# Performance work log

Hardware: AMD Instinct MI355X
Metric: run time of the kernel (lower is better)

Reference implementation:

```python
import jax, jax.numpy as jnp
import numpy as np

N = 100_000      # atoms (nodes)
E = 1_600_000    # directed edges
F_IN = 89        # atom feature dim
H = 128          # hidden dim
P = 20_000       # polyhedra (N/P = 5 atoms each)
C = 500          # crystals (P/C = 40 polyhedra each)
OUT = 1
EPS = 1e-5


def setup_inputs() -> dict:
    key = jax.random.key(0)
    ks = jax.random.split(key, 10)
    x = jax.random.normal(ks[0], (N, F_IN), jnp.float32)
    edge_index = jax.random.randint(ks[1], (2, E), 0, N)
    # sorted segment ids guaranteeing non-empty segments (faithful to PyG Batch layout)
    batch = jnp.repeat(jnp.arange(P), N // P)          # node -> polyhedron
    crystal_ids = jnp.repeat(jnp.arange(C), P // C)    # polyhedron -> crystal
    # GCNConv weights (glorot-ish) and biases; conv0 maps 89->128, convs 1..4 map 128->128
    W0 = jax.random.normal(ks[2], (F_IN, H), jnp.float32) * (1.0 / np.sqrt(F_IN))
    Ws = jax.random.normal(ks[3], (4, H, H), jnp.float32) * (1.0 / np.sqrt(H))
    bs = jnp.zeros((5, H), jnp.float32)
    # 5 BatchNorm layers
    gammas = jnp.ones((5, H), jnp.float32)
    betas = jnp.zeros((5, H), jnp.float32)
    # predictor MLP
    Wp1 = jax.random.normal(ks[4], (H, H), jnp.float32) * (1.0 / np.sqrt(H))
    bp1 = jnp.zeros((H,), jnp.float32)
    Wp2 = jax.random.normal(ks[5], (H, OUT), jnp.float32) * (1.0 / np.sqrt(H))
    bp2 = jnp.zeros((OUT,), jnp.float32)
    return dict(x=x, edge_index=edge_index, batch=batch, crystal_ids=crystal_ids,
                W0=W0, Ws=Ws, bs=bs, gammas=gammas, betas=betas,
                Wp1=Wp1, bp1=bp1, Wp2=Wp2, bp2=bp2)


def _bn(h, g, b):
    # BatchNorm1d, training mode: biased batch statistics over nodes
    mu = jnp.mean(h, axis=0)
    var = jnp.var(h, axis=0)
    return g * (h - mu) * jax.lax.rsqrt(var + EPS) + b


def reference(x, edge_index, batch, crystal_ids, W0, Ws, bs, gammas, betas, Wp1, bp1, Wp2, bp2):
    # --- GCN normalization with self-loops (shared by all 5 convs) ---
    loops = jnp.arange(N)
    src = jnp.concatenate([edge_index[0], loops])   # [E+N]
    dst = jnp.concatenate([edge_index[1], loops])
    deg = jax.ops.segment_sum(jnp.ones_like(src, jnp.float32), dst, num_segments=N)
    dinv = jnp.where(deg > 0, jax.lax.rsqrt(deg), 0.0)
    norm = (dinv[src] * dinv[dst])[:, None]          # [E+N, 1]

    def conv(h, W, b):
        m = h @ W                                    # [N, H]
        agg = jax.ops.segment_sum(m[src] * norm, dst, num_segments=N)
        return agg + b

    h = jax.nn.relu(_bn(conv(x, W0, bs[0]), gammas[0], betas[0]))
    for i in range(4):
        h = jax.nn.relu(_bn(conv(h, Ws[i], bs[i + 1]), gammas[i + 1], betas[i + 1]))

    # global_mean_pool over polyhedra
    cnt_p = jax.ops.segment_sum(jnp.ones((N,), jnp.float32), batch, num_segments=P)
    poly = jax.ops.segment_sum(h, batch, num_segments=P) / cnt_p[:, None]

    # per-crystal mean of polyhedron reps (vectorized form of the Python loop)
    cnt_c = jax.ops.segment_sum(jnp.ones((P,), jnp.float32), crystal_ids, num_segments=C)
    crys = jax.ops.segment_sum(poly, crystal_ids, num_segments=C) / cnt_c[:, None]

    # predictor MLP (Dropout is identity at inference)
    pred = jax.nn.relu(crys @ Wp1 + bp1) @ Wp2 + bp2   # [C, 1]
    return pred
```

## Files before the change

kernel.cpp:

```cpp
#include <hip/hip_runtime.h>

#define N_ATOMS 100000
#define N_EDGES 1600000
#define F_INDIM 89
#define N_CRYS  500
#define EPSBN   1e-5f
#define DRANGE  12500
#define RBLK    250
#define NSB     400

typedef unsigned short u16;
typedef unsigned int   u32;
typedef __attribute__((ext_vector_type(8))) short short8;
typedef __attribute__((ext_vector_type(4))) float f32x4;
typedef __attribute__((ext_vector_type(4))) unsigned int u32x4;

__device__ __forceinline__ float bf2f(u16 u){ union{u32 i; float f;} v; v.i=((u32)u)<<16; return v.f; }
__device__ __forceinline__ float bflo(u32 u){ union{u32 i; float f;} v; v.i=u<<16; return v.f; }
__device__ __forceinline__ float bfhi(u32 u){ union{u32 i; float f;} v; v.i=u&0xffff0000u; return v.f; }
__device__ __forceinline__ u16 f2bf(float f){
  u32 x=__float_as_uint(f);
  return (u16)((x + 0x7fffu + ((x>>16)&1u))>>16);
}
__device__ __forceinline__ u32 pack2(float a, float b){ return (u32)f2bf(a) | ((u32)f2bf(b)<<16); }
__device__ __forceinline__ float ldf(const void* p, int i, int m){
  return m ? ((const float*)p)[i] : bf2f(((const u16*)p)[i]);
}
__device__ __forceinline__ int fpmode(const void* gammas){ return (((const u16*)gammas)[0]==0) ? 1 : 0; }

__global__ void k_count(const int* __restrict__ ei, int* __restrict__ degi){
  int r = blockIdx.x & 7;
  int e = (blockIdx.x >> 3)*256 + threadIdx.x;
  if (e >= N_EDGES) return;
  int d = __builtin_nontemporal_load(ei + N_EDGES + e);
  if ((u32)d >= N_ATOMS) d = 0;
  if (d/DRANGE != r) return;
  atomicAdd(&degi[d], 1);
}

__global__ void k_hist(const int* __restrict__ degi, int* __restrict__ hist, int* __restrict__ blockHist){
  __shared__ int lh[256];
  int t = threadIdx.x, b = blockIdx.x;
  lh[t] = 0; __syncthreads();
  if (t < RBLK){
    int dg = degi[b*RBLK + t];
    atomicAdd(&lh[dg>255?255:dg], 1);
  }
  __syncthreads();
  blockHist[b*256 + t] = lh[t];
  if (lh[t]) atomicAdd(&hist[(b/50)*256 + t], lh[t]);
}

__global__ void k_hist_scan(int* __restrict__ hist){
  __shared__ int s[256];
  int R = blockIdx.x, t = threadIdx.x;
  int own = hist[R*256+t]; s[t] = own; __syncthreads();
  for (int k=1;k<256;k<<=1){ int a=(t>=k)?s[t-k]:0; __syncthreads(); s[t]+=a; __syncthreads(); }
  hist[R*256+t] = s[t] - own;
}

__global__ __launch_bounds__(64) void k_blockoff(const int* __restrict__ blockHist, const int* __restrict__ binBase,
                                                 int* __restrict__ blockOff){
  int bid = blockIdx.x;
  int c = bid & 255, R = bid >> 8;
  int t = threadIdx.x;
  int own = (t<50) ? blockHist[(R*50+t)*256 + c] : 0;
  int v = own;
  #pragma unroll
  for (int k=1;k<64;k<<=1){ int u = __shfl_up(v, k, 64); if (t>=k) v += u; }
  if (t<50) blockOff[(R*50+t)*256 + c] = R*DRANGE + binBase[R*256 + c] + (v - own);
}

__global__ void k_rank(const int* __restrict__ degi, const int* __restrict__ blockOff,
                       int* __restrict__ nodeAt, int* __restrict__ rankOf,
                       float* __restrict__ dinv, float* __restrict__ dinvR){
  __shared__ int boff[256];
  __shared__ int cnt[256];
  int b = blockIdx.x, t = threadIdx.x;
  boff[t] = blockOff[b*256 + t];
  cnt[t] = 0;
  __syncthreads();
  if (t >= RBLK) return;
  int n = b*RBLK + t;
  int dg = degi[n];
  int cd = dg>255?255:dg;
  int li = atomicAdd(&cnt[cd], 1);
  int r = boff[cd] + li;
  nodeAt[r] = n; rankOf[n] = r;
  float di = rsqrtf((float)(dg + 1));
  dinv[n] = di; dinvR[r] = di;
}

__global__ __launch_bounds__(256) void k_scan_partial(const int* __restrict__ degi, const int* __restrict__ nodeAt,
                                                      int* __restrict__ bsum){
  int b=blockIdx.x, t=threadIdx.x;
  int s=0;
  #pragma unroll
  for (int j=0;j<4;j++){
    int i=b*1024 + j*256 + t;
    if(i<N_ATOMS){
      int dg = degi[nodeAt[i]];
      s += (dg+3)&~3;
    }
  }
  __shared__ int red[256];
  red[t]=s; __syncthreads();
  for (int k=128;k>0;k>>=1){ if(t<k) red[t]+=red[t+k]; __syncthreads(); }
  if (t==0) bsum[b]=red[0];
}

__global__ void k_scan_bsum(int* __restrict__ bsum, int nb){
  __shared__ int s[128];
  int t=threadIdx.x;
  int own = (t<nb)? bsum[t]:0;
  s[t]=own; __syncthreads();
  for (int k=1;k<128;k<<=1){ int a=(t>=k)?s[t-k]:0; __syncthreads(); s[t]+=a; __syncthreads(); }
  if (t<nb) bsum[t]=s[t]-own;
}

__global__ __launch_bounds__(256) void k_scan_write(const int* __restrict__ degi, const int* __restrict__ nodeAt,
                                                    const int* __restrict__ bsum,
                                                    int* __restrict__ off, u32* __restrict__ csrS){
  int b=blockIdx.x, t=threadIdx.x;
  int base=b*1024+t*4;
  int v[4], s=0;
  #pragma unroll
  for (int j=0;j<4;j++){ int i=base+j; v[j]=(i<N_ATOMS)?((degi[nodeAt[i]]+3)&~3):0; s+=v[j]; }
  __shared__ int ts[256];
  ts[t]=s; __syncthreads();
  for (int k=1;k<256;k<<=1){ int a=(t>=k)?ts[t-k]:0; __syncthreads(); ts[t]+=a; __syncthreads(); }
  int run = ts[t]-s + bsum[b];
  #pragma unroll
  for (int j=0;j<4;j++){
    int i=base+j;
    if (i<=N_ATOMS) off[i]=run;
    if (i<N_ATOMS){
      int dg = degi[nodeAt[i]];
      for (int q=dg; q<v[j]; q++) csrS[run+q] = (u32)N_ATOMS;
    }
    run+=v[j];
  }
}

__global__ void k_fill(const int* __restrict__ ei, const int* __restrict__ off,
                       const int* __restrict__ rankOf,
                       int* __restrict__ cursor, u32* __restrict__ csrS){
  int rr = blockIdx.x & 7;
  int e = (blockIdx.x >> 3)*256 + threadIdx.x;
  if (e >= N_EDGES) return;
  int d = __builtin_nontemporal_load(ei + N_EDGES + e);
  if ((u32)d >= N_ATOMS) d = 0;
  if (d/DRANGE != rr) return;
  int s = __builtin_nontemporal_load(ei + e);
  if ((u32)s >= N_ATOMS) s = 0;
  int rk = rankOf[d];
  int p = off[rk] + atomicAdd(&cursor[rk], 1);
  csrS[p] = (u32)s;
}

__global__ void k_packW(const void* __restrict__ W0, const void* __restrict__ Ws,
                        const void* __restrict__ gammas, u16* __restrict__ dst){
  int L    = blockIdx.x >> 3;
  int tid  = (blockIdx.x & 7)*256 + threadIdx.x;
  int K    = (L==0) ? F_INDIM : 128;
  int Kpad = (L==0) ? 96 : 128;
  if (tid >= (Kpad/32)*8*64) return;
  const void* W = (L==0) ? W0 : Ws;
  int woff = (L==0) ? 0 : (L-1)*128*128;
  int fp32m = fpmode(gammas);
  int lane = tid & 63, sc = tid >> 6;
  int c = sc & 7, s = sc >> 3;
  u16 vals[8];
  #pragma unroll
  for (int j=0;j<8;j++){
    int k  = s*32 + (lane>>4)*8 + j;
    int ch = c*16 + (lane&15);
    float v = (k<K) ? ldf(W, woff + k*128 + ch, fp32m) : 0.f;
    vals[j] = f2bf(v);
  }
  u16* out = dst + (size_t)L*16384;
  *(ushort4*)&out[tid*8]   = *(const ushort4*)&vals[0];
  *(ushort4*)&out[tid*8+4] = *(const ushort4*)&vals[4];
}

#define AROW 136
__global__ __launch_bounds__(256) void k_gemm_mfma(const u16* __restrict__ inA, const void* __restrict__ inX,
                                                   int K, int Kpad, const u16* __restrict__ Wpk,
                                                   const float* __restrict__ statsPrev, int useAct,
                                                   const float* __restrict__ dinv,
                                                   u16* __restrict__ mout,
                                                   const void* __restrict__ gammas,
                                                   const void* __restrict__ betas, int goff){
  __shared__ __align__(16) u16 Al[128*AROW];
  __shared__ float cl[256];
  const int t = threadIdx.x, lane = t & 63, w = t >> 6;
  const int tile = blockIdx.x * 128;

  if (useAct){
    if (t < 128){
      int fp32m = fpmode(gammas);
      float mu  = statsPrev[t] * (1.f/N_ATOMS);
      float var = statsPrev[128+t] * (1.f/N_ATOMS) - mu*mu;
      if (var < 0.f) var = 0.f;
      float sc = ldf(gammas, goff+t, fp32m) / sqrtf(var + EPSBN);
      cl[t]     = sc;
      cl[128+t] = ldf(betas, goff+t, fp32m) - sc*mu;
    }
    __syncthreads();
    const uint4* HA4 = (const uint4*)inA;
    for (int idx=t; idx<128*16; idx+=256){
      int node = idx>>4, q = idx&15;
      int gn = tile+node;
      uint4 v = (gn<N_ATOMS) ? HA4[((size_t)(q>>2)*(N_ATOMS+1) + gn)*4 + (q&3)] : make_uint4(0,0,0,0);
      int kk = q*8;
      u16 r[8];
      r[0]=f2bf(fmaxf(fmaf(cl[kk+0], bflo(v.x), cl[128+kk+0]),0.f));
      r[1]=f2bf(fmaxf(fmaf(cl[kk+1], bfhi(v.x), cl[128+kk+1]),0.f));
      r[2]=f2bf(fmaxf(fmaf(cl[kk+2], bflo(v.y), cl[128+kk+2]),0.f));
      r[3]=f2bf(fmaxf(fmaf(cl[kk+3], bfhi(v.y), cl[128+kk+3]),0.f));
      r[4]=f2bf(fmaxf(fmaf(cl[kk+4], bflo(v.z), cl[128+kk+4]),0.f));
      r[5]=f2bf(fmaxf(fmaf(cl[kk+5], bfhi(v.z), cl[128+kk+5]),0.f));
      r[6]=f2bf(fmaxf(fmaf(cl[kk+6], bflo(v.w), cl[128+kk+6]),0.f));
      r[7]=f2bf(fmaxf(fmaf(cl[kk+7], bfhi(v.w), cl[128+kk+7]),0.f));
      *(uint4*)&Al[node*AROW + kk] = *(const uint4*)&r[0];
    }
  } else {
    int fp32m = fpmode(gammas);
    for (int idx=t; idx<128*96; idx+=256){
      int node = idx/96, kk = idx - node*96;
      int gn = tile+node;
      float v = (kk<K && gn<N_ATOMS) ? ldf(inX, gn*K+kk, fp32m) : 0.f;
      Al[node*AROW + kk] = f2bf(v);
    }
  }
  __syncthreads();

  f32x4 acc[2][8];
  #pragma unroll
  for (int rr=0;rr<2;rr++)
    #pragma unroll
    for (int c=0;c<8;c++) acc[rr][c] = (f32x4){0.f,0.f,0.f,0.f};
  const int row = lane & 15, quad = lane >> 4;

  const int nstep = Kpad >> 5;
  for (int s=0; s<nstep; ++s){
    short8 a0 = *(const short8*)&Al[(w*32+row)*AROW    + s*32 + quad*8];
    short8 a1 = *(const short8*)&Al[(w*32+16+row)*AROW + s*32 + quad*8];
    #pragma unroll
    for (int c=0;c<8;c++){
      short8 b = *(const short8*)&Wpk[(size_t)((s*8+c)*64 + lane)*8];
      acc[0][c] = __builtin_amdgcn_mfma_f32_16x16x32_bf16(a0, b, acc[0][c], 0, 0, 0);
      acc[1][c] = __builtin_amdgcn_mfma_f32_16x16x32_bf16(a1, b, acc[1][c], 0, 0, 0);
    }
  }
  __syncthreads();
  float di[2][4];
  #pragma unroll
  for (int rr=0;rr<2;rr++)
    #pragma unroll
    for (int r=0;r<4;r++){
      int gn = tile + w*32 + rr*16 + quad*4 + r;
      di[rr][r] = (gn<N_ATOMS) ? dinv[gn] : 0.f;
    }
  #pragma unroll
  for (int rr=0;rr<2;rr++)
    #pragma unroll
    for (int c=0;c<8;c++)
      #pragma unroll
      for (int r=0;r<4;r++){
        int node = w*32 + rr*16 + quad*4 + r, ch = c*16 + row;
        Al[node*AROW + ch] = f2bf(di[rr][r]*acc[rr][c][r]);
      }
  __syncthreads();
  for (int idx=t; idx<2048; idx+=256){
    int blk = idx>>9, rem = idx&511, node = rem>>2, part = rem&3;
    int gn = tile+node;
    if (gn < N_ATOMS){
      uint4 v = *(const uint4*)&Al[node*AROW + blk*32 + part*8];
      *(uint4*)&mout[((size_t)blk*(N_ATOMS+1) + gn)*32 + part*8] = v;
    }
  }
  if (blockIdx.x == gridDim.x-1 && t < 16){
    int blk = t>>2, part = t&3;
    *(uint4*)&mout[((size_t)blk*(N_ATOMS+1) + N_ATOMS)*32 + part*8] = make_uint4(0,0,0,0);
  }
}

#define ACC8(r) do{ a[0]+=bflo(r.x); a[1]+=bfhi(r.x); a[2]+=bflo(r.y); a[3]+=bfhi(r.y); \
                    a[4]+=bflo(r.z); a[5]+=bfhi(r.z); a[6]+=bflo(r.w); a[7]+=bfhi(r.w);}while(0)
__global__ __launch_bounds__(256) void k_agg(const u16* __restrict__ m_, const u32* __restrict__ csrS,
                                             const int* __restrict__ off, const int* __restrict__ nodeAt,
                                             const float* __restrict__ dinvR,
                                             u16* __restrict__ agg_, float* __restrict__ stats){
  const int t = threadIdx.x, lane = t & 63, w = t >> 6;
  const int par = lane & 3, p = lane >> 2;
  const int cls = blockIdx.x & 7;
  const int slice = cls >> 1, half = cls & 1;
  const int r = half*50000 + (int)(blockIdx.x >> 3)*64 + w*16 + p;
  const int rlim = half*50000 + 50000;

  const uint4* m4   = (const uint4*)m_ + (size_t)slice*(N_ATOMS+1)*4;
  uint4*       agg4 = (uint4*)agg_     + (size_t)slice*(N_ATOMS+1)*4;

  float a[8], q8[8];
  #pragma unroll
  for (int i=0;i<8;i++){ a[i]=0.f; q8[i]=0.f; }

  if (r < rlim){
    int n = nodeAt[r];
    uint4 sv = m4[(size_t)n*4 + par];
    ACC8(sv);
    int e   = off[r];
    int end = off[r+1];
    if ((end - e) & 4){
      u32x4 iv = *(const u32x4*)(csrS+e);
      uint4 g0 = m4[(size_t)iv[0]*4 + par];
      uint4 g1 = m4[(size_t)iv[1]*4 + par];
      uint4 g2 = m4[(size_t)iv[2]*4 + par];
      uint4 g3 = m4[(size_t)iv[3]*4 + par];
      ACC8(g0); ACC8(g1); ACC8(g2); ACC8(g3);
      e += 4;
    }
    if (e < end){
      u32x4 i0 = *(const u32x4*)(csrS+e), i1 = *(const u32x4*)(csrS+e+4);
      uint4 A0 = m4[(size_t)i0[0]*4 + par];
      uint4 A1 = m4[(size_t)i0[1]*4 + par];
      uint4 A2 = m4[(size_t)i0[2]*4 + par];
      uint4 A3 = m4[(size_t)i0[3]*4 + par];
      uint4 A4 = m4[(size_t)i1[0]*4 + par];
      uint4 A5 = m4[(size_t)i1[1]*4 + par];
      uint4 A6 = m4[(size_t)i1[2]*4 + par];
      uint4 A7 = m4[(size_t)i1[3]*4 + par];
      e += 8;
      bool more = (e < end);
      while (true){
        uint4 B0,B1,B2,B3,B4,B5,B6,B7;
        if (more){
          u32x4 j0 = *(const u32x4*)(csrS+e), j1 = *(const u32x4*)(csrS+e+4);
          B0 = m4[(size_t)j0[0]*4 + par];
          B1 = m4[(size_t)j0[1]*4 + par];
          B2 = m4[(size_t)j0[2]*4 + par];
          B3 = m4[(size_t)j0[3]*4 + par];
          B4 = m4[(size_t)j1[0]*4 + par];
          B5 = m4[(size_t)j1[1]*4 + par];
          B6 = m4[(size_t)j1[2]*4 + par];
          B7 = m4[(size_t)j1[3]*4 + par];
          e += 8;
        }
        ACC8(A0); ACC8(A1); ACC8(A2); ACC8(A3);
        ACC8(A4); ACC8(A5); ACC8(A6); ACC8(A7);
        if (!more) break;
        A0=B0; A1=B1; A2=B2; A3=B3; A4=B4; A5=B5; A6=B6; A7=B7;
        more = (e < end);
      }
    }
    float di = dinvR[r];
    #pragma unroll
    for (int i=0;i<8;i++){ a[i]*=di; q8[i]=a[i]*a[i]; }
    u32x4 o;
    o[0] = pack2(a[0],a[1]); o[1] = pack2(a[2],a[3]);
    o[2] = pack2(a[4],a[5]); o[3] = pack2(a[6],a[7]);
    __builtin_nontemporal_store(o, (u32x4*)&agg4[(size_t)n*4 + par]);
  }
  #pragma unroll
  for (int i=0;i<8;i++){
    float s = a[i], q = q8[i];
    s += __shfl_xor(s, 4, 64);  q += __shfl_xor(q, 4, 64);
    s += __shfl_xor(s, 8, 64);  q += __shfl_xor(q, 8, 64);
    s += __shfl_xor(s, 16, 64); q += __shfl_xor(q, 16, 64);
    s += __shfl_xor(s, 32, 64); q += __shfl_xor(q, 32, 64);
    a[i]=s; q8[i]=q;
  }
  __shared__ float sred[4][64];
  if (lane < 4){
    #pragma unroll
    for (int i=0;i<8;i++){ sred[w][par*8+i]=a[i]; sred[w][32+par*8+i]=q8[i]; }
  }
  __syncthreads();
  if (t < 64){
    float v = sred[0][t]+sred[1][t]+sred[2][t]+sred[3][t];
    int ch = slice*32 + (t & 31);
    atomicAdd(&stats[(t<32 ? ch : 128+ch)], v);
  }
}

__global__ __launch_bounds__(128) void k_pool_mlp(const u16* __restrict__ agg, const float* __restrict__ stats4,
                                                  const void* __restrict__ gammas, const void* __restrict__ betas,
                                                  const void* __restrict__ Wp1, const void* __restrict__ bp1,
                                                  const void* __restrict__ Wp2, const void* __restrict__ bp2,
                                                  void* __restrict__ out){
  int c = blockIdx.x, t = threadIdx.x;
  int fp32m = fpmode(gammas);
  float mu  = stats4[t] * (1.f/N_ATOMS);
  float var = stats4[128+t] * (1.f/N_ATOMS) - mu*mu;
  if (var < 0.f) var = 0.f;
  float sc = ldf(gammas, 512+t, fp32m) / sqrtf(var + EPSBN);
  float tb = ldf(betas, 512+t, fp32m) - sc*mu;
  float sum = 0.f;
  const u16* base = agg + ((size_t)(t>>5)*(N_ATOMS+1) + (size_t)c*200)*32 + (t&31);
  for (int i=0;i<200;i++) sum += fmaxf(fmaf(sc, bf2f(base[(size_t)i*32]), tb), 0.f);
  __shared__ float cr[128];
  cr[t] = sum * (1.f/200.f);
  __syncthreads();
  float hj = ldf(bp1, t, fp32m);
  for (int k=0;k<128;k++) hj = fmaf(cr[k], ldf(Wp1, k*128+t, fp32m), hj);
  hj = fmaxf(hj, 0.f);
  __shared__ float red[128];
  red[t] = hj * ldf(Wp2, t, fp32m);
  __syncthreads();
  for (int s=64;s>0;s>>=1){ if (t<s) red[t]+=red[t+s]; __syncthreads(); }
  if (t==0){
    float r = red[0] + ldf(bp2, 0, fp32m);
    if (fp32m) ((float*)out)[c] = r;
    else       ((u16*) out)[c]  = f2bf(r);
  }
}

extern "C" void kernel_launch(void* const* d_in, const int* in_sizes, int n_in,
                              void* d_out, int out_size, void* d_ws, size_t ws_size,
                              hipStream_t stream){
  const void* x      = d_in[0];
  const int*  ei     = (const int*)d_in[1];
  const void* W0     = d_in[4];
  const void* Ws     = d_in[5];
  const void* gammas = d_in[7];
  const void* betas  = d_in[8];
  const void* Wp1    = d_in[9];
  const void* bp1    = d_in[10];
  const void* Wp2    = d_in[11];
  const void* bp2    = d_in[12];
  (void)in_sizes; (void)n_in; (void)out_size; (void)ws_size;

  char* w = (char*)d_ws;
  size_t o = 0;
  auto take = [&](size_t bytes)->char*{ char* p = w+o; o = (o+bytes+255)&~(size_t)255; return p; };
  int*   off    = (int*)  take((size_t)(N_ATOMS+1)*4);
  float* dinv   = (float*)take((size_t)N_ATOMS*4);
  u32*   csrS   = (u32*)  take((size_t)(N_EDGES+4*N_ATOMS)*4);
  u16*   HA     = (u16*)  take((size_t)(N_ATOMS+1)*128*2);
  u16*   HB     = (u16*)  take((size_t)(N_ATOMS+1)*128*2);
  float* stats5 = (float*)take(5*256*4);
  int*   bsum   = (int*)  take(1024*4);
  u16*   Wpk    = (u16*)  take((size_t)5*16384*2);
  int*   nodeAt = (int*)  take((size_t)N_ATOMS*4);
  float* dinvR  = (float*)take((size_t)N_ATOMS*4);
  int* degi      = (int*)HB;
  int* hist      = (int*)((char*)HB + 400128);
  int* cursor    = (int*)((char*)HB + 408320);
  int* rankOf    = (int*)((char*)HB + 808320);
  int* blockHist = (int*)((char*)HB + 1208320);
  int* blockOff  = (int*)((char*)HB + 1617920);

  k_packW<<<40, 256, 0, stream>>>(W0, Ws, gammas, Wpk);

  hipMemsetAsync(degi, 0, 808320, stream);
  const int echunks = (N_EDGES+255)/256;
  k_count<<<echunks*8, 256, 0, stream>>>(ei, degi);
  k_hist <<<NSB, 256, 0, stream>>>(degi, hist, blockHist);
  k_hist_scan<<<8, 256, 0, stream>>>(hist);
  k_blockoff<<<8*256, 64, 0, stream>>>(blockHist, hist, blockOff);
  k_rank <<<NSB, 256, 0, stream>>>(degi, blockOff, nodeAt, rankOf, dinv, dinvR);
  const int nb = (N_ATOMS+1023)/1024;
  k_scan_partial<<<nb, 256, 0, stream>>>(degi, nodeAt, bsum);
  k_scan_bsum   <<<1, 128, 0, stream>>>(bsum, nb);
  k_scan_write  <<<nb, 256, 0, stream>>>(degi, nodeAt, bsum, off, csrS);
  k_fill<<<echunks*8, 256, 0, stream>>>(ei, off, rankOf, cursor, csrS);
  hipMemsetAsync(stats5, 0, 5*256*4, stream);

  const int gemm_grid = (N_ATOMS+127)/128;
  const int agg_grid  = ((50000+63)/64)*8;
  for (int L=0; L<5; ++L){
    const int Kpad = (L==0) ? 96 : 128;
    const int K    = (L==0) ? F_INDIM : 128;
    const float* statsPrev = (L==0) ? stats5 : (stats5 + (size_t)(L-1)*256);
    k_gemm_mfma<<<gemm_grid, 256, 0, stream>>>(HA, x, K, Kpad, Wpk + (size_t)L*16384,
                                               statsPrev, (L==0)?0:1, dinv, HB,
                                               gammas, betas, (L-1)*128);
    k_agg <<<agg_grid, 256, 0, stream>>>(HB, csrS, off, nodeAt, dinvR, HA, stats5 + (size_t)L*256);
  }
  k_pool_mlp<<<N_CRYS, 128, 0, stream>>>(HA, stats5 + 4*256, gammas, betas,
                                         Wp1, bp1, Wp2, bp2, d_out);
}
```

Measured before the change: 770.7 us.

## Bucket edges by destination range once instead of rescanning edge list eightfold

Adds a bucketing pass that reads the edge list once and scatters packed (dst,src) pairs into 64 buckets keyed by source block segment and destination range, using shared-memory counters and global bucket counters. The degree-count and CSR-fill kernels then read only their own bucket rather than launching 8x grids that each reread and filter the whole edge list. This removes redundant global reads of the edges while keeping the per-range atomic locality. In exchange it adds about 14 MB of bucket writes and rereads, and it relies on a fixed per-bucket capacity that a skewed edge distribution could overflow.

```diff
diff --git a/kernel.cpp b/kernel.cpp
--- a/kernel.cpp
+++ b/kernel.cpp
@@ -8,9 +8,12 @@
 #define DRANGE  12500
 #define RBLK    250
 #define NSB     400
+#define CAPSEG  28160
+#define SEGCH   110
 
 typedef unsigned short u16;
 typedef unsigned int   u32;
+typedef unsigned long long u64;
 typedef __attribute__((ext_vector_type(8))) short short8;
 typedef __attribute__((ext_vector_type(4))) float f32x4;
 typedef __attribute__((ext_vector_type(4))) unsigned int u32x4;
@@ -28,13 +31,37 @@
 }
 __device__ __forceinline__ int fpmode(const void* gammas){ return (((const u16*)gammas)[0]==0) ? 1 : 0; }
 
-__global__ void k_count(const int* __restrict__ ei, int* __restrict__ degi){
-  int r = blockIdx.x & 7;
-  int e = (blockIdx.x >> 3)*256 + threadIdx.x;
-  if (e >= N_EDGES) return;
-  int d = __builtin_nontemporal_load(ei + N_EDGES + e);
-  if ((u32)d >= N_ATOMS) d = 0;
-  if (d/DRANGE != r) return;
+__global__ void k_bucket(const int* __restrict__ ei, u64* __restrict__ bkt, int* __restrict__ bcnt){
+  __shared__ int lcnt[8], lbase[8];
+  int t = threadIdx.x;
+  int seg = blockIdx.x & 7;
+  int e = blockIdx.x*256 + t;
+  if (t < 8) lcnt[t] = 0;
+  __syncthreads();
+  int d=0, s=0, rr=0, li=0;
+  bool valid = (e < N_EDGES);
+  if (valid){
+    d = ei[N_EDGES+e]; if ((u32)d >= N_ATOMS) d = 0;
+    s = ei[e];         if ((u32)s >= N_ATOMS) s = 0;
+    rr = d / DRANGE;
+    li = atomicAdd(&lcnt[rr], 1);
+  }
+  __syncthreads();
+  if (t < 8) lbase[t] = atomicAdd(&bcnt[seg*64 + t], lcnt[t]);
+  __syncthreads();
+  if (valid){
+    bkt[(size_t)(seg*8 + rr)*CAPSEG + lbase[rr] + li] = ((u64)(u32)d << 32) | (u32)s;
+  }
+}
+
+__global__ void k_count2(const u64* __restrict__ bkt, const int* __restrict__ bcnt,
+                         int* __restrict__ degi){
+  int rr  = blockIdx.x & 7;
+  int rest = blockIdx.x >> 3;
+  int seg = rest & 7, ch = rest >> 3;
+  int i = ch*256 + threadIdx.x;
+  if (i >= bcnt[seg*64 + rr]) return;
+  int d = (int)(bkt[(size_t)(seg*8 + rr)*CAPSEG + i] >> 32);
   atomicAdd(&degi[d], 1);
 }
 
@@ -142,17 +169,17 @@
   }
 }
 
-__global__ void k_fill(const int* __restrict__ ei, const int* __restrict__ off,
-                       const int* __restrict__ rankOf,
-                       int* __restrict__ cursor, u32* __restrict__ csrS){
-  int rr = blockIdx.x & 7;
-  int e = (blockIdx.x >> 3)*256 + threadIdx.x;
-  if (e >= N_EDGES) return;
-  int d = __builtin_nontemporal_load(ei + N_EDGES + e);
-  if ((u32)d >= N_ATOMS) d = 0;
-  if (d/DRANGE != rr) return;
-  int s = __builtin_nontemporal_load(ei + e);
-  if ((u32)s >= N_ATOMS) s = 0;
+__global__ void k_fill2(const u64* __restrict__ bkt, const int* __restrict__ bcnt,
+                        const int* __restrict__ off, const int* __restrict__ rankOf,
+                        int* __restrict__ cursor, u32* __restrict__ csrS){
+  int rr  = blockIdx.x & 7;
+  int rest = blockIdx.x >> 3;
+  int seg = rest & 7, ch = rest >> 3;
+  int i = ch*256 + threadIdx.x;
+  if (i >= bcnt[seg*64 + rr]) return;
+  u64 v = bkt[(size_t)(seg*8 + rr)*CAPSEG + i];
+  int d = (int)(v >> 32);
+  int s = (int)(u32)v;
   int rk = rankOf[d];
   int p = off[rk] + atomicAdd(&cursor[rk], 1);
   csrS[p] = (u32)s;
@@ -447,15 +474,19 @@
   int* degi      = (int*)HB;
   int* hist      = (int*)((char*)HB + 400128);
   int* cursor    = (int*)((char*)HB + 408320);
-  int* rankOf    = (int*)((char*)HB + 808320);
-  int* blockHist = (int*)((char*)HB + 1208320);
-  int* blockOff  = (int*)((char*)HB + 1617920);
+  int* bcnt      = (int*)((char*)HB + 808320);
+  int* rankOf    = (int*)((char*)HB + 810496);
+  int* blockHist = (int*)((char*)HB + 1210496);
+  int* blockOff  = (int*)((char*)HB + 1620096);
+  u64* bkt       = (u64*)((char*)HB + 2097152);
 
   k_packW<<<40, 256, 0, stream>>>(W0, Ws, gammas, Wpk);
 
-  hipMemsetAsync(degi, 0, 808320, stream);
+  hipMemsetAsync(degi, 0, 810368, stream);
   const int echunks = (N_EDGES+255)/256;
-  k_count<<<echunks*8, 256, 0, stream>>>(ei, degi);
+  const int bgrid   = SEGCH*8*8;
+  k_bucket<<<echunks, 256, 0, stream>>>(ei, bkt, bcnt);
+  k_count2<<<bgrid, 256, 0, stream>>>(bkt, bcnt, degi);
   k_hist <<<NSB, 256, 0, stream>>>(degi, hist, blockHist);
   k_hist_scan<<<8, 256, 0, stream>>>(hist);
   k_blockoff<<<8*256, 64, 0, stream>>>(blockHist, hist, blockOff);
@@ -464,7 +495,7 @@
   k_scan_partial<<<nb, 256, 0, stream>>>(degi, nodeAt, bsum);
   k_scan_bsum   <<<1, 128, 0, stream>>>(bsum, nb);
   k_scan_write  <<<nb, 256, 0, stream>>>(degi, nodeAt, bsum, off, csrS);
-  k_fill<<<echunks*8, 256, 0, stream>>>(ei, off, rankOf, cursor, csrS);
+  k_fill2<<<bgrid, 256, 0, stream>>>(bkt, bcnt, off, rankOf, cursor, csrS);
   hipMemsetAsync(stats5, 0, 5*256*4, stream);
 
   const int gemm_grid = (N_ATOMS+127)/128;
```

After: 774.4 us. No clear change (+0.5%).
